# Performance work log

Measured on AMD Instinct MI355X. Metric: run time of the kernel, lower is better.

The kernel has to match this reference:

```python
import jax, jax.numpy as jnp
import numpy as np

N_HEADS, INPUT_DIM, EMBED_DIM = 8, 512, 512
KEY_DIM = EMBED_DIM // N_HEADS  # val_dim == key_dim == 64


def _uniform(key, shape, stdv):
    return jax.random.uniform(key, shape, jnp.float32, -stdv, stdv)


def setup_inputs() -> dict:
    key = jax.random.key(0)
    kh, kq, kk, kv, ko = jax.random.split(key, 5)
    stdv_qkv = 1.0 / np.sqrt(KEY_DIM)
    stdv_out = 1.0 / np.sqrt(EMBED_DIM)
    return {
        "h": jax.random.normal(kh, (4, 2048, INPUT_DIM), jnp.float32),
        "W_query": _uniform(kq, (N_HEADS, INPUT_DIM, KEY_DIM), stdv_qkv),
        "W_key": _uniform(kk, (N_HEADS, INPUT_DIM, KEY_DIM), stdv_qkv),
        "W_val": _uniform(kv, (N_HEADS, INPUT_DIM, KEY_DIM), stdv_qkv),
        "W_out": _uniform(ko, (N_HEADS * KEY_DIM, EMBED_DIM), stdv_out),
    }


def reference(h, W_query, W_key, W_val, W_out):
    # h: [b, n, d_in]; W_{q,k,v}: [H, d_in, dk]; W_out: [H*dk, d_model]
    norm = 1.0 / np.sqrt(KEY_DIM)
    Q = jnp.einsum('bnd,hdk->hbnk', h, W_query)
    K = jnp.einsum('bnd,hdk->hbnk', h, W_key)
    V = jnp.einsum('bnd,hdk->hbnk', h, W_val)
    compat = norm * jnp.einsum('hbnk,hbmk->hbnm', Q, K)  # [H,b,n,n]
    attn = jax.nn.softmax(compat, axis=-1)
    heads = jnp.einsum('hbnm,hbmk->hbnk', attn, V)        # [H,b,n,dk]
    b, n = h.shape[0], h.shape[1]
    heads = jnp.transpose(heads, (1, 2, 0, 3)).reshape(b, n, N_HEADS * KEY_DIM)
    return heads @ W_out
```

## Files before the change

### kernel.cpp

```cpp
#include <hip/hip_runtime.h>
#include <hip/hip_bf16.h>
#include <hip/hip_fp16.h>

#define H 8
#define B 4
#define NSEQ 2048
#define DIN 512
#define DK 64
#define DMODEL 512
#define ROWS (B*NSEQ)

typedef _Float16 f16x8 __attribute__((ext_vector_type(8)));
typedef _Float16 f16x4 __attribute__((ext_vector_type(4)));
typedef float f32x4 __attribute__((ext_vector_type(4)));
typedef unsigned u32x4 __attribute__((ext_vector_type(4)));

#define EXP2F(x) __builtin_amdgcn_exp2f(x)

#define AS1(p) ((const __attribute__((address_space(1))) void*)(const void*)(p))
#define AS3(p) ((__attribute__((address_space(3))) void*)(void*)(p))

static __device__ __forceinline__ unsigned pk16(float a, float b) {
    auto h = __builtin_amdgcn_cvt_pkrtz(a, b);
    return __builtin_bit_cast(unsigned, h);
}

__global__ void k_prep(const float* __restrict__ Wq,
                       const float* __restrict__ Wk,
                       const float* __restrict__ Wv,
                       const float* __restrict__ Wo,
                       _Float16* __restrict__ Wt,
                       _Float16* __restrict__ Wot)
{
    const long nw = (long)3 * H * DK * DIN;
    const long no = (long)DMODEL * DMODEL;
    const long total = nw + no;
    for (long i = (long)blockIdx.x * blockDim.x + threadIdx.x; i < total;
         i += (long)gridDim.x * blockDim.x) {
        if (i < nw) {
            int j = (int)i;
            int m   = j / (H * DK * DIN);
            int rem = j % (H * DK * DIN);
            int hh  = rem / (DK * DIN);
            int r2  = rem % (DK * DIN);
            int c   = r2 / DIN;
            int d   = r2 % DIN;
            const float* W = (m == 0) ? Wq : ((m == 1) ? Wk : Wv);
            Wt[j] = (_Float16)W[hh * DIN * DK + d * DK + c];
        } else {
            int j = (int)(i - nw);
            int e = j / DMODEL;
            int c = j % DMODEL;
            Wot[j] = (_Float16)Wo[c * DMODEL + e];
        }
    }
}

__global__ __launch_bounds__(256, 3) void k_qkv(
    const float*    __restrict__ h,
    const _Float16* __restrict__ Wt,
    _Float16* __restrict__ Qs,
    _Float16* __restrict__ Kb,
    _Float16* __restrict__ Vt)
{
    const int rt = blockIdx.x;
    const int ct = blockIdx.y;
    const int t  = threadIdx.x;
    const int w  = t >> 6;
    const int l  = t & 63;
    const int l15 = l & 15, lg = l >> 4;
    const int wr = w >> 1, wc = w & 1;

    __shared__ _Float16 Al[2][128*32];
    __shared__ _Float16 Bl[2][128*32];

    const int srow  = l >> 2;
    const int schnk = (l & 3) ^ (srow & 3);
    const float*    asrc = h  + (long)(rt*128 + w*16 + srow)*DIN + schnk*8;
    const _Float16* bsrc = Wt + (long)(ct*128 + w*16 + srow)*DIN + schnk*8;

    float4 ar[4];
    auto aload = [&](int kt) {
        const float* a0 = asrc + kt*32;
        ar[0] = *(const float4*)(a0);
        ar[1] = *(const float4*)(a0 + 4);
        ar[2] = *(const float4*)(a0 + 64*DIN);
        ar[3] = *(const float4*)(a0 + 64*DIN + 4);
    };
    auto awrite = [&](int bufi) {
        u32x4 v0, v1;
        v0[0] = pk16(ar[0].x, ar[0].y); v0[1] = pk16(ar[0].z, ar[0].w);
        v0[2] = pk16(ar[1].x, ar[1].y); v0[3] = pk16(ar[1].z, ar[1].w);
        v1[0] = pk16(ar[2].x, ar[2].y); v1[1] = pk16(ar[2].z, ar[2].w);
        v1[2] = pk16(ar[3].x, ar[3].y); v1[3] = pk16(ar[3].z, ar[3].w);
        *(u32x4*)&Al[bufi][w*512 + l*8]        = v0;
        *(u32x4*)&Al[bufi][2048 + w*512 + l*8] = v1;
    };
    auto bstage = [&](int kt, int bufi) {
        const _Float16* bs = bsrc + kt*32;
        __builtin_amdgcn_global_load_lds(AS1(bs),          AS3(&Bl[bufi][w*512]),        16, 0, 0);
        __builtin_amdgcn_global_load_lds(AS1(bs + 64*DIN), AS3(&Bl[bufi][2048 + w*512]), 16, 0, 0);
    };

    f32x4 acc[4][4] = {};

    aload(0); awrite(0); bstage(0, 0);
    __syncthreads();

    const int co = (lg ^ (l15 & 3)) * 8;
    for (int kt = 0; kt < 16; ++kt) {
        const int cur = kt & 1;
        if (kt + 1 < 16) { aload(kt + 1); bstage(kt + 1, cur ^ 1); }

        f16x8 af[4], bf[4];
#pragma unroll
        for (int am = 0; am < 4; ++am)
            af[am] = *(const f16x8*)&Al[cur][(wr*64 + am*16 + l15)*32 + co];
#pragma unroll
        for (int an = 0; an < 4; ++an)
            bf[an] = *(const f16x8*)&Bl[cur][(wc*64 + an*16 + l15)*32 + co];
#pragma unroll
        for (int am = 0; am < 4; ++am)
#pragma unroll
            for (int an = 0; an < 4; ++an)
                acc[am][an] = __builtin_amdgcn_mfma_f32_16x16x32_f16(af[am], bf[an], acc[am][an], 0, 0, 0);

        if (kt + 1 < 16) awrite(cur ^ 1);
        __syncthreads();
    }

    const int m = (ct*128) >> 9;
    const float QSCALE = 0.125f * 1.44269504088896f;
#pragma unroll
    for (int an = 0; an < 4; ++an) {
        const int col = ct*128 + wc*64 + an*16 + l15;
        const int hd = (col >> 6) & 7, dk = col & 63;
#pragma unroll
        for (int am = 0; am < 4; ++am) {
            const int rowb = rt*128 + wr*64 + am*16 + lg*4;
            const int b = rowb >> 11, n = rowb & 2047;
            const long p = (long)hd*B + b;
            if (m == 0) {
#pragma unroll
                for (int r = 0; r < 4; ++r)
                    Qs[(p*NSEQ + n + r)*DK + dk] = (_Float16)(acc[am][an][r] * QSCALE);
            } else if (m == 1) {
#pragma unroll
                for (int r = 0; r < 4; ++r)
                    Kb[(p*NSEQ + n + r)*DK + dk] = (_Float16)acc[am][an][r];
            } else {
                const int u0 = n & 63;
                const int fu = u0 >> 4, lgu = (u0 >> 2) & 3;
                const int tcol = (n & ~63) + (fu & 1)*32 + lgu*8 + (fu >> 1)*4;
                f16x4 pk;
                pk[0] = (_Float16)acc[am][an][0]; pk[1] = (_Float16)acc[am][an][1];
                pk[2] = (_Float16)acc[am][an][2]; pk[3] = (_Float16)acc[am][an][3];
                *(f16x4*)&Vt[(p*DK + dk)*NSEQ + tcol] = pk;
            }
        }
    }
}

__global__ __launch_bounds__(256, 4) void k_attn(
    const _Float16* __restrict__ Qs,
    const _Float16* __restrict__ Kb,
    const _Float16* __restrict__ Vt,
    _Float16* __restrict__ heads)
{
    const int bid = blockIdx.x;
    const int xcd = bid & 7, slot = bid >> 3;
    const int p   = (xcd << 2) | (slot >> 5);
    const int qt  = slot & 31;
    const int t = threadIdx.x, w = t >> 6, l = t & 63;
    const int l15 = l & 15, lg = l >> 4;

    __shared__ _Float16 Kl[2][64][64];
    __shared__ _Float16 Vl[2][64][64];

    const _Float16* Qp = Qs + (long)p*NSEQ*DK;
    const _Float16* Kp = Kb + (long)p*NSEQ*DK;
    const _Float16* Vp = Vt + (long)p*DK*NSEQ;

    const int qrow = qt*64 + w*16;
    const f16x8 qa0 = *(const f16x8*)(Qp + (long)(qrow + l15)*DK + 8*lg);
    const f16x8 qa1 = *(const f16x8*)(Qp + (long)(qrow + l15)*DK + 32 + 8*lg);

    const float M0 = 20.0f;
    float lrun = 0.f;
    f32x4 acco[4] = {};

    const int rsub = l >> 3;
    const int csw  = (l & 7) ^ rsub;
    auto stage = [&](int kt, int bufi) {
        const long kb = (long)kt * 64;
        __builtin_amdgcn_global_load_lds(
            AS1(Kp + (kb + w*16     + rsub)*DK + csw*8),
            AS3(&Kl[bufi][w*16][0]),     16, 0, 0);
        __builtin_amdgcn_global_load_lds(
            AS1(Kp + (kb + w*16 + 8 + rsub)*DK + csw*8),
            AS3(&Kl[bufi][w*16 + 8][0]), 16, 0, 0);
        __builtin_amdgcn_global_load_lds(
            AS1(Vp + (long)(w*16     + rsub)*NSEQ + kb + csw*8),
            AS3(&Vl[bufi][w*16][0]),     16, 0, 0);
        __builtin_amdgcn_global_load_lds(
            AS1(Vp + (long)(w*16 + 8 + rsub)*NSEQ + kb + csw*8),
            AS3(&Vl[bufi][w*16 + 8][0]), 16, 0, 0);
    };

    stage(0, 0);
    __syncthreads();

    for (int kt = 0; kt < 32; ++kt) {
        const int cur = kt & 1;
        if (kt + 1 < 32) stage(kt + 1, cur ^ 1);

        const char* kbase = (const char*)&Kl[cur][0][0];
        f32x4 st[4];
#pragma unroll
        for (int f = 0; f < 4; ++f) { st[f][0] = -M0; st[f][1] = -M0; st[f][2] = -M0; st[f][3] = -M0; }
        __builtin_amdgcn_s_setprio(1);
#pragma unroll
        for (int f = 0; f < 4; ++f) {
            const int row = f*16 + l15;
            const int sw  = l15 & 7;
            f16x8 k0 = *(const f16x8*)(kbase + row*128 + ((lg     ^ sw)*16));
            f16x8 k1 = *(const f16x8*)(kbase + row*128 + (((4+lg) ^ sw)*16));
            st[f] = __builtin_amdgcn_mfma_f32_16x16x32_f16(k0, qa0, st[f], 0, 0, 0);
            st[f] = __builtin_amdgcn_mfma_f32_16x16x32_f16(k1, qa1, st[f], 0, 0, 0);
        }
        __builtin_amdgcn_s_setprio(0);

        float sf[4];
#pragma unroll
        for (int f = 0; f < 4; ++f) {
#pragma unroll
            for (int r = 0; r < 4; ++r) st[f][r] = EXP2F(st[f][r]);
            sf[f] = (st[f][0] + st[f][1]) + (st[f][2] + st[f][3]);
        }
        lrun += (sf[0] + sf[1]) + (sf[2] + sf[3]);

        u32x4 paw[2];
#pragma unroll
        for (int kk = 0; kk < 2; ++kk) {
            u32x4 v4;
            v4[0] = pk16(st[kk][0],   st[kk][1]);
            v4[1] = pk16(st[kk][2],   st[kk][3]);
            v4[2] = pk16(st[kk+2][0], st[kk+2][1]);
            v4[3] = pk16(st[kk+2][2], st[kk+2][3]);
            paw[kk] = v4;
        }

        const char* vbase = (const char*)&Vl[cur][0][0];
        __builtin_amdgcn_s_setprio(1);
#pragma unroll
        for (int kk = 0; kk < 2; ++kk) {
            const f16x8 pa = __builtin_bit_cast(f16x8, paw[kk]);
#pragma unroll
            for (int g = 0; g < 4; ++g) {
                const int row = g*16 + l15;
                const int ch  = (kk*4 + lg) ^ (l15 & 7);
                f16x8 vf = *(const f16x8*)(vbase + row*128 + ch*16);
                acco[g] = __builtin_amdgcn_mfma_f32_16x16x32_f16(pa, vf, acco[g], 0, 0, 0);
            }
        }
        __builtin_amdgcn_s_setprio(0);

        __syncthreads();
    }

    const int hd = p >> 2, b = p & 3;
    lrun += __shfl_xor(lrun, 16);
    lrun += __shfl_xor(lrun, 32);
    const int rbase = qrow + lg*4;
#pragma unroll
    for (int r = 0; r < 4; ++r) {
        const float inv = 1.f / __shfl(lrun, lg*4 + r);
        const int n = rbase + r;
        const long rowoff = ((long)b*NSEQ + n)*DMODEL + hd*64;
#pragma unroll
        for (int g = 0; g < 4; ++g)
            heads[rowoff + g*16 + l15] = (_Float16)(acco[g][r] * inv);
    }
}

__global__ __launch_bounds__(256, 4) void k_out(
    const _Float16* __restrict__ heads,
    const _Float16* __restrict__ Wot,
    float* __restrict__ out)
{
    const int rt = blockIdx.x;
    const int ct = blockIdx.y;
    const int t = threadIdx.x, w = t >> 6, l = t & 63;
    const int l15 = l & 15, lg = l >> 4;
    const int wr = w >> 1, wc = w & 1;

    __shared__ _Float16 Al[2][128*32];
    __shared__ _Float16 Bl[2][128*32];

    const int srow  = l >> 2;
    const int schnk = (l & 3) ^ (srow & 3);
    const _Float16* asrc = heads + (long)(rt*128 + w*16 + srow)*DMODEL + schnk*8;
    const _Float16* bsrc = Wot   + (long)(ct*128 + w*16 + srow)*DMODEL + schnk*8;

    auto stage = [&](int kt, int bufi) {
        const _Float16* as = asrc + kt*32;
        const _Float16* bs = bsrc + kt*32;
        __builtin_amdgcn_global_load_lds(AS1(as),             AS3(&Al[bufi][w*512]),        16, 0, 0);
        __builtin_amdgcn_global_load_lds(AS1(as + 64*DMODEL), AS3(&Al[bufi][2048 + w*512]), 16, 0, 0);
        __builtin_amdgcn_global_load_lds(AS1(bs),             AS3(&Bl[bufi][w*512]),        16, 0, 0);
        __builtin_amdgcn_global_load_lds(AS1(bs + 64*DMODEL), AS3(&Bl[bufi][2048 + w*512]), 16, 0, 0);
    };

    f32x4 acc[4][4] = {};

    stage(0, 0);
    __syncthreads();

    const int co = (lg ^ (l15 & 3)) * 8;
    for (int kt = 0; kt < 16; ++kt) {
        const int cur = kt & 1;
        if (kt + 1 < 16) stage(kt + 1, cur ^ 1);

        f16x8 af[4], bf[4];
#pragma unroll
        for (int am = 0; am < 4; ++am)
            af[am] = *(const f16x8*)&Al[cur][(wr*64 + am*16 + l15)*32 + co];
#pragma unroll
        for (int an = 0; an < 4; ++an)
            bf[an] = *(const f16x8*)&Bl[cur][(wc*64 + an*16 + l15)*32 + co];
#pragma unroll
        for (int am = 0; am < 4; ++am)
#pragma unroll
            for (int an = 0; an < 4; ++an)
                acc[am][an] = __builtin_amdgcn_mfma_f32_16x16x32_f16(af[am], bf[an], acc[am][an], 0, 0, 0);

        __syncthreads();
    }

#pragma unroll
    for (int an = 0; an < 4; ++an) {
        const int col = ct*128 + wc*64 + an*16 + l15;
#pragma unroll
        for (int am = 0; am < 4; ++am) {
            const int rowb = rt*128 + wr*64 + am*16 + lg*4;
#pragma unroll
            for (int r = 0; r < 4; ++r)
                out[(long)(rowb + r)*DMODEL + col] = acc[am][an][r];
        }
    }
}

extern "C" void kernel_launch(void* const* d_in, const int* in_sizes, int n_in,
                              void* d_out, int out_size, void* d_ws, size_t ws_size,
                              hipStream_t stream) {
    const float* h  = (const float*)d_in[0];
    const float* Wq = (const float*)d_in[1];
    const float* Wk = (const float*)d_in[2];
    const float* Wv = (const float*)d_in[3];
    const float* Wo = (const float*)d_in[4];
    float* out = (float*)d_out;

    char* ws = (char*)d_ws;
    _Float16* heads = (_Float16*)ws;  ws += (size_t)ROWS*DMODEL*2;
    _Float16* Wt    = (_Float16*)ws;  ws += (size_t)3*H*DK*DIN*2;
    _Float16* Wot   = (_Float16*)ws;  ws += (size_t)DMODEL*DMODEL*2;
    _Float16* Qs    = (_Float16*)ws;  ws += (size_t)H*B*NSEQ*DK*2;
    _Float16* Kb    = (_Float16*)ws;  ws += (size_t)H*B*NSEQ*DK*2;
    _Float16* Vt    = (_Float16*)ws;  ws += (size_t)H*B*NSEQ*DK*2;

    k_prep<<<dim3(512),    dim3(256), 0, stream>>>(Wq, Wk, Wv, Wo, Wt, Wot);
    k_qkv <<<dim3(64, 12), dim3(256), 0, stream>>>(h, Wt, Qs, Kb, Vt);
    k_attn<<<dim3(1024),   dim3(256), 0, stream>>>(Qs, Kb, Vt, heads);
    k_out <<<dim3(64, 4),  dim3(256), 0, stream>>>(heads, Wot, out);
}
```

Baseline: 97.56 us.

## Split attention KV range in two, double query rows per warp, merge in out-proj

The attention kernel now processes 32 query rows per warp (two 16-row groups) over half of the key sequence. Each K/V tile loaded into LDS is reused across twice as many queries, and the block count stays the same. The two partial unnormalized outputs and row sums are written to workspace, and the output projection loads both partials, adds them, divides by the summed denominators, and writes the fp16 A tile into LDS through registers instead of async global-to-LDS copies. This relies on the fixed max offset in the softmax so partials can be summed directly, and it adds extra global traffic for the doubled partial output plus register pressure in the attention loop.

```diff
diff --git a/kernel.cpp b/kernel.cpp
--- a/kernel.cpp
+++ b/kernel.cpp
@@ -165,12 +165,15 @@
     const _Float16* __restrict__ Qs,
     const _Float16* __restrict__ Kb,
     const _Float16* __restrict__ Vt,
-    _Float16* __restrict__ heads)
+    _Float16* __restrict__ Opart,
+    float*    __restrict__ Lsum)
 {
     const int bid = blockIdx.x;
     const int xcd = bid & 7, slot = bid >> 3;
     const int p   = (xcd << 2) | (slot >> 5);
-    const int qt  = slot & 31;
+    const int rem = slot & 31;
+    const int qt  = rem >> 1;
+    const int sp  = rem & 1;
     const int t = threadIdx.x, w = t >> 6, l = t & 63;
     const int l15 = l & 15, lg = l >> 4;
 
@@ -181,13 +184,17 @@
     const _Float16* Kp = Kb + (long)p*NSEQ*DK;
     const _Float16* Vp = Vt + (long)p*DK*NSEQ;
 
-    const int qrow = qt*64 + w*16;
-    const f16x8 qa0 = *(const f16x8*)(Qp + (long)(qrow + l15)*DK + 8*lg);
-    const f16x8 qa1 = *(const f16x8*)(Qp + (long)(qrow + l15)*DK + 32 + 8*lg);
+    const int qrow = qt*128 + w*32;
+    f16x8 qa[2][2];
+#pragma unroll
+    for (int G = 0; G < 2; ++G) {
+        qa[G][0] = *(const f16x8*)(Qp + (long)(qrow + G*16 + l15)*DK + 8*lg);
+        qa[G][1] = *(const f16x8*)(Qp + (long)(qrow + G*16 + l15)*DK + 32 + 8*lg);
+    }
 
     const float M0 = 20.0f;
-    float lrun = 0.f;
-    f32x4 acco[4] = {};
+    float lrun[2] = {0.f, 0.f};
+    f32x4 acco[2][4] = {};
 
     const int rsub = l >> 3;
     const int csw  = (l & 7) ^ rsub;
@@ -207,17 +214,23 @@
             AS3(&Vl[bufi][w*16 + 8][0]), 16, 0, 0);
     };
 
-    stage(0, 0);
+    const int kt0 = sp * 16;
+    stage(kt0, 0);
     __syncthreads();
 
-    for (int kt = 0; kt < 32; ++kt) {
-        const int cur = kt & 1;
-        if (kt + 1 < 32) stage(kt + 1, cur ^ 1);
+    for (int i = 0; i < 16; ++i) {
+        const int cur = i & 1;
+        if (i + 1 < 16) stage(kt0 + i + 1, cur ^ 1);
 
         const char* kbase = (const char*)&Kl[cur][0][0];
-        f32x4 st[4];
-#pragma unroll
-        for (int f = 0; f < 4; ++f) { st[f][0] = -M0; st[f][1] = -M0; st[f][2] = -M0; st[f][3] = -M0; }
+        f32x4 st[2][4];
+#pragma unroll
+        for (int G = 0; G < 2; ++G)
+#pragma unroll
+            for (int f = 0; f < 4; ++f) {
+                st[G][f][0] = -M0; st[G][f][1] = -M0;
+                st[G][f][2] = -M0; st[G][f][3] = -M0;
+            }
         __builtin_amdgcn_s_setprio(1);
 #pragma unroll
         for (int f = 0; f < 4; ++f) {
@@ -225,42 +238,51 @@
             const int sw  = l15 & 7;
             f16x8 k0 = *(const f16x8*)(kbase + row*128 + ((lg     ^ sw)*16));
             f16x8 k1 = *(const f16x8*)(kbase + row*128 + (((4+lg) ^ sw)*16));
-            st[f] = __builtin_amdgcn_mfma_f32_16x16x32_f16(k0, qa0, st[f], 0, 0, 0);
-            st[f] = __builtin_amdgcn_mfma_f32_16x16x32_f16(k1, qa1, st[f], 0, 0, 0);
+            st[0][f] = __builtin_amdgcn_mfma_f32_16x16x32_f16(k0, qa[0][0], st[0][f], 0, 0, 0);
+            st[0][f] = __builtin_amdgcn_mfma_f32_16x16x32_f16(k1, qa[0][1], st[0][f], 0, 0, 0);
+            st[1][f] = __builtin_amdgcn_mfma_f32_16x16x32_f16(k0, qa[1][0], st[1][f], 0, 0, 0);
+            st[1][f] = __builtin_amdgcn_mfma_f32_16x16x32_f16(k1, qa[1][1], st[1][f], 0, 0, 0);
         }
         __builtin_amdgcn_s_setprio(0);
 
-        float sf[4];
-#pragma unroll
-        for (int f = 0; f < 4; ++f) {
-#pragma unroll
-            for (int r = 0; r < 4; ++r) st[f][r] = EXP2F(st[f][r]);
-            sf[f] = (st[f][0] + st[f][1]) + (st[f][2] + st[f][3]);
-        }
-        lrun += (sf[0] + sf[1]) + (sf[2] + sf[3]);
-
-        u32x4 paw[2];
-#pragma unroll
-        for (int kk = 0; kk < 2; ++kk) {
-            u32x4 v4;
-            v4[0] = pk16(st[kk][0],   st[kk][1]);
-            v4[1] = pk16(st[kk][2],   st[kk][3]);
-            v4[2] = pk16(st[kk+2][0], st[kk+2][1]);
-            v4[3] = pk16(st[kk+2][2], st[kk+2][3]);
-            paw[kk] = v4;
-        }
+#pragma unroll
+        for (int G = 0; G < 2; ++G) {
+            float sf[4];
+#pragma unroll
+            for (int f = 0; f < 4; ++f) {
+#pragma unroll
+                for (int r = 0; r < 4; ++r) st[G][f][r] = EXP2F(st[G][f][r]);
+                sf[f] = (st[G][f][0] + st[G][f][1]) + (st[G][f][2] + st[G][f][3]);
+            }
+            lrun[G] += (sf[0] + sf[1]) + (sf[2] + sf[3]);
+        }
+
+        u32x4 paw[2][2];
+#pragma unroll
+        for (int G = 0; G < 2; ++G)
+#pragma unroll
+            for (int kk = 0; kk < 2; ++kk) {
+                u32x4 v4;
+                v4[0] = pk16(st[G][kk][0],   st[G][kk][1]);
+                v4[1] = pk16(st[G][kk][2],   st[G][kk][3]);
+                v4[2] = pk16(st[G][kk+2][0], st[G][kk+2][1]);
+                v4[3] = pk16(st[G][kk+2][2], st[G][kk+2][3]);
+                paw[G][kk] = v4;
+            }
 
         const char* vbase = (const char*)&Vl[cur][0][0];
         __builtin_amdgcn_s_setprio(1);
 #pragma unroll
         for (int kk = 0; kk < 2; ++kk) {
-            const f16x8 pa = __builtin_bit_cast(f16x8, paw[kk]);
+            const f16x8 pa0 = __builtin_bit_cast(f16x8, paw[0][kk]);
+            const f16x8 pa1 = __builtin_bit_cast(f16x8, paw[1][kk]);
 #pragma unroll
             for (int g = 0; g < 4; ++g) {
                 const int row = g*16 + l15;
                 const int ch  = (kk*4 + lg) ^ (l15 & 7);
                 f16x8 vf = *(const f16x8*)(vbase + row*128 + ch*16);
-                acco[g] = __builtin_amdgcn_mfma_f32_16x16x32_f16(pa, vf, acco[g], 0, 0, 0);
+                acco[0][g] = __builtin_amdgcn_mfma_f32_16x16x32_f16(pa0, vf, acco[0][g], 0, 0, 0);
+                acco[1][g] = __builtin_amdgcn_mfma_f32_16x16x32_f16(pa1, vf, acco[1][g], 0, 0, 0);
             }
         }
         __builtin_amdgcn_s_setprio(0);
@@ -269,22 +291,29 @@
     }
 
     const int hd = p >> 2, b = p & 3;
-    lrun += __shfl_xor(lrun, 16);
-    lrun += __shfl_xor(lrun, 32);
-    const int rbase = qrow + lg*4;
-#pragma unroll
-    for (int r = 0; r < 4; ++r) {
-        const float inv = 1.f / __shfl(lrun, lg*4 + r);
-        const int n = rbase + r;
-        const long rowoff = ((long)b*NSEQ + n)*DMODEL + hd*64;
-#pragma unroll
-        for (int g = 0; g < 4; ++g)
-            heads[rowoff + g*16 + l15] = (_Float16)(acco[g][r] * inv);
+    _Float16* Op = Opart + (long)sp * ROWS * DMODEL;
+    float*    Lp = Lsum  + (long)sp * 32 * NSEQ + (long)p * NSEQ;
+#pragma unroll
+    for (int G = 0; G < 2; ++G) {
+        lrun[G] += __shfl_xor(lrun[G], 16);
+        lrun[G] += __shfl_xor(lrun[G], 32);
+        if (lg == 0) Lp[qrow + G*16 + l15] = lrun[G];
+        const int rbase = qrow + G*16 + lg*4;
+#pragma unroll
+        for (int r = 0; r < 4; ++r) {
+            const int n = rbase + r;
+            const long rowoff = ((long)b*NSEQ + n)*DMODEL + hd*64;
+#pragma unroll
+            for (int g = 0; g < 4; ++g)
+                Op[rowoff + g*16 + l15] = (_Float16)acco[G][g][r];
+        }
     }
 }
 
 __global__ __launch_bounds__(256, 4) void k_out(
-    const _Float16* __restrict__ heads,
+    const _Float16* __restrict__ O0,
+    const _Float16* __restrict__ O1,
+    const float*    __restrict__ Ls,
     const _Float16* __restrict__ Wot,
     float* __restrict__ out)
 {
@@ -299,27 +328,53 @@
 
     const int srow  = l >> 2;
     const int schnk = (l & 3) ^ (srow & 3);
-    const _Float16* asrc = heads + (long)(rt*128 + w*16 + srow)*DMODEL + schnk*8;
-    const _Float16* bsrc = Wot   + (long)(ct*128 + w*16 + srow)*DMODEL + schnk*8;
-
-    auto stage = [&](int kt, int bufi) {
-        const _Float16* as = asrc + kt*32;
+    const int row0 = rt*128 + w*16 + srow;
+    const int row1 = row0 + 64;
+    const int bb   = row0 >> 11;
+    const int n0   = row0 & 2047, n1 = row1 & 2047;
+    const _Float16* bsrc = Wot + (long)(ct*128 + w*16 + srow)*DMODEL + schnk*8;
+    const float* L1p = Ls + 32*NSEQ;
+
+    f16x8 oa0, oa1, ob0, ob1;
+    float inva, invb;
+    auto aload = [&](int kt) {
+        const long c = (long)kt*32 + schnk*8;
+        oa0 = *(const f16x8*)(O0 + (long)row0*DMODEL + c);
+        oa1 = *(const f16x8*)(O1 + (long)row0*DMODEL + c);
+        ob0 = *(const f16x8*)(O0 + (long)row1*DMODEL + c);
+        ob1 = *(const f16x8*)(O1 + (long)row1*DMODEL + c);
+        const int hd = kt >> 1;
+        const long pl = (long)(hd*B + bb) * NSEQ;
+        inva = 1.f / (Ls[pl + n0] + L1p[pl + n0]);
+        invb = 1.f / (Ls[pl + n1] + L1p[pl + n1]);
+    };
+    auto awrite = [&](int bufi) {
+        u32x4 v0, v1;
+#pragma unroll
+        for (int j = 0; j < 4; ++j) {
+            v0[j] = pk16(((float)oa0[2*j]   + (float)oa1[2*j])   * inva,
+                         ((float)oa0[2*j+1] + (float)oa1[2*j+1]) * inva);
+            v1[j] = pk16(((float)ob0[2*j]   + (float)ob1[2*j])   * invb,
+                         ((float)ob0[2*j+1] + (float)ob1[2*j+1]) * invb);
+        }
+        *(u32x4*)&Al[bufi][w*512 + l*8]        = v0;
+        *(u32x4*)&Al[bufi][2048 + w*512 + l*8] = v1;
+    };
+    auto bstage = [&](int kt, int bufi) {
         const _Float16* bs = bsrc + kt*32;
-        __builtin_amdgcn_global_load_lds(AS1(as),             AS3(&Al[bufi][w*512]),        16, 0, 0);
-        __builtin_amdgcn_global_load_lds(AS1(as + 64*DMODEL), AS3(&Al[bufi][2048 + w*512]), 16, 0, 0);
         __builtin_amdgcn_global_load_lds(AS1(bs),             AS3(&Bl[bufi][w*512]),        16, 0, 0);
         __builtin_amdgcn_global_load_lds(AS1(bs + 64*DMODEL), AS3(&Bl[bufi][2048 + w*512]), 16, 0, 0);
     };
 
     f32x4 acc[4][4] = {};
 
-    stage(0, 0);
+    aload(0); awrite(0); bstage(0, 0);
     __syncthreads();
 
     const int co = (lg ^ (l15 & 3)) * 8;
     for (int kt = 0; kt < 16; ++kt) {
         const int cur = kt & 1;
-        if (kt + 1 < 16) stage(kt + 1, cur ^ 1);
+        if (kt + 1 < 16) { aload(kt + 1); bstage(kt + 1, cur ^ 1); }
 
         f16x8 af[4], bf[4];
 #pragma unroll
@@ -334,6 +389,7 @@
             for (int an = 0; an < 4; ++an)
                 acc[am][an] = __builtin_amdgcn_mfma_f32_16x16x32_f16(af[am], bf[an], acc[am][an], 0, 0, 0);
 
+        if (kt + 1 < 16) awrite(cur ^ 1);
         __syncthreads();
     }
 
@@ -361,15 +417,17 @@
     float* out = (float*)d_out;
 
     char* ws = (char*)d_ws;
-    _Float16* heads = (_Float16*)ws;  ws += (size_t)ROWS*DMODEL*2;
     _Float16* Wt    = (_Float16*)ws;  ws += (size_t)3*H*DK*DIN*2;
     _Float16* Wot   = (_Float16*)ws;  ws += (size_t)DMODEL*DMODEL*2;
     _Float16* Qs    = (_Float16*)ws;  ws += (size_t)H*B*NSEQ*DK*2;
     _Float16* Kb    = (_Float16*)ws;  ws += (size_t)H*B*NSEQ*DK*2;
     _Float16* Vt    = (_Float16*)ws;  ws += (size_t)H*B*NSEQ*DK*2;
+    _Float16* Opart = (_Float16*)ws;  ws += (size_t)2*ROWS*DMODEL*2;
+    float*    Lsum  = (float*)ws;     ws += (size_t)2*32*NSEQ*4;
 
     k_prep<<<dim3(512),    dim3(256), 0, stream>>>(Wq, Wk, Wv, Wo, Wt, Wot);
     k_qkv <<<dim3(64, 12), dim3(256), 0, stream>>>(h, Wt, Qs, Kb, Vt);
-    k_attn<<<dim3(1024),   dim3(256), 0, stream>>>(Qs, Kb, Vt, heads);
-    k_out <<<dim3(64, 4),  dim3(256), 0, stream>>>(heads, Wot, out);
-}
+    k_attn<<<dim3(1024),   dim3(256), 0, stream>>>(Qs, Kb, Vt, Opart, Lsum);
+    k_out <<<dim3(64, 4),  dim3(256), 0, stream>>>(Opart, Opart + (size_t)ROWS*DMODEL,
+                                                   Lsum, Wot, out);
+}
```

After: 98.75 us. About the same (+1.2%).
